# Optimization experiments

Measured on AMD Instinct MI355X. Metric: run time of the kernel, lower is better.

The kernel has to match this reference:

```python
import jax, jax.numpy as jnp
import numpy as np
from jax import lax

T = 0.2  # temperature

def _l2norm(x, axis):
    n = jnp.sqrt(jnp.sum(x * x, axis=axis, keepdims=True))
    return x / jnp.maximum(n, 1e-12)

def setup_inputs() -> dict:
    key = jax.random.key(0)
    k1, k2, k3, k4 = jax.random.split(key, 4)
    B, K, C, H, W, Q = 16, 5, 256, 128, 128, 64
    res1 = jax.random.normal(k1, (B, K, H, W), jnp.float32)
    fea1 = jax.random.normal(k2, (B, C, H, W), jnp.float32)
    gt = jax.random.randint(k3, (B, H, W), 0, K, dtype=jnp.int32)
    # queue buffers, L2-normalized along feature dim (torch normalize(dim=0) on [C,Q])
    queues = _l2norm(jax.random.normal(k4, (K, C, Q), jnp.float32), axis=1)
    return {"res1": res1, "fea1": fea1, "queues": queues, "gt": gt, "label_bs": 8}

def reference(res1, fea1, queues, gt, label_bs):
    B, K, H, W = res1.shape
    C = fea1.shape[1]
    HW = H * W
    # per-sample prediction: gt for labeled samples, argmax of logits otherwise
    pred_arg = jnp.argmax(res1, axis=1).reshape(B, HW)
    pred_gt = gt.reshape(B, HW).astype(pred_arg.dtype)
    labeled = (jnp.arange(B) < label_bs)[:, None]
    pred = jnp.where(labeled, pred_gt, pred_arg)  # [B, HW]

    fea = fea1.reshape(B, C, HW)
    # masked segment-mean per class (vectorized version of the per-unique-label loop)
    onehot = (pred[:, None, :] == jnp.arange(K)[None, :, None]).astype(fea.dtype)  # [B,K,HW]
    counts = onehot.sum(-1)                                    # [B,K]
    sums = jnp.einsum('bkp,bcp->bkc', onehot, fea)             # [B,K,C]
    means = sums / jnp.maximum(counts, 1.0)[..., None]
    keys_all = _l2norm(means, axis=-1)                         # [B,K,C]

    present = counts > 0                                       # [B,K]
    # Faithful replication of the source's off-by-one: keys[list(vals).index(c)]
    # selects the mean of the PREVIOUS present class (vals excludes the smallest
    # present label while keys keeps all unique labels in sorted order).
    idx = jnp.where(present, jnp.arange(K)[None, :], -1)
    cmax = lax.cummax(idx, axis=1)
    prev = jnp.concatenate([jnp.full((B, 1), -1, cmax.dtype), cmax[:, :-1]], axis=1)  # [B,K]
    smallest = jnp.argmax(present, axis=1)                     # first present class
    valid = present & (jnp.arange(K)[None, :] != smallest[:, None]) & (prev >= 0)

    query = jnp.take_along_axis(keys_all, jnp.maximum(prev, 0)[:, :, None], axis=1)  # [B,K,C]

    qd = lax.stop_gradient(queues)  # queues are detached buffers in the original
    sim = jnp.einsum('bkc,jcq->bkjq', query, qd) / T           # [B,K,K,Q]
    l_pos = jnp.einsum('bkc,kcq->bkq', query, qd) / T          # [B,K,Q]
    sumE = jnp.exp(sim).sum(-1)                                # [B,K,K]
    off = 1.0 - jnp.eye(K, dtype=sumE.dtype)
    neg = (sumE * off[None]).sum(-1)                           # [B,K] cross-class negatives
    l_neg = jnp.exp(l_pos) + neg[:, :, None]                   # [B,K,Q]
    log_prob = (l_pos - jnp.log(l_neg)).mean(-1)               # [B,K]

    loss_c = jnp.where(valid, -log_prob, 0.0)
    n_present = present.sum(1)
    denom = n_present - 1  # len(vals)
    per_sample = jnp.where(denom > 0, loss_c.sum(1) / jnp.maximum(denom, 1), 0.0)
    return per_sample.sum() / B
```

## Files before the change

kernel.cpp:

```cpp
#include <hip/hip_runtime.h>
#include <cstddef>

constexpr int B_  = 16;
constexpr int K_  = 5;
constexpr int C_  = 256;
constexpr int HW_ = 128 * 128;
constexpr int Q_  = 64;
constexpr float T_ = 0.2f;

typedef float f4 __attribute__((ext_vector_type(4)));

__global__ __launch_bounds__(256) void pred_kernel(
    const float* __restrict__ res1, const int* __restrict__ gt,
    const int* __restrict__ label_bs, unsigned int* __restrict__ predp)
{
    int idx = blockIdx.x * 256 + threadIdx.x;
    int b  = idx >> 12;
    int p4 = idx & 4095;
    int lb = label_bs[0];
    unsigned int packed;
    if (b < lb) {
        int4 g = reinterpret_cast<const int4*>(gt + (size_t)b * HW_)[p4];
        packed = (unsigned)(g.x & 0xFF) | ((unsigned)(g.y & 0xFF) << 8)
               | ((unsigned)(g.z & 0xFF) << 16) | ((unsigned)(g.w & 0xFF) << 24);
    } else {
        const float4* r = reinterpret_cast<const float4*>(res1 + (size_t)b * K_ * HW_) + p4;
        float4 best = r[0];
        int a0 = 0, a1 = 0, a2 = 0, a3 = 0;
        #pragma unroll
        for (int k = 1; k < K_; ++k) {
            float4 v = r[(size_t)k * (HW_ / 4)];
            if (v.x > best.x) { best.x = v.x; a0 = k; }
            if (v.y > best.y) { best.y = v.y; a1 = k; }
            if (v.z > best.z) { best.z = v.z; a2 = k; }
            if (v.w > best.w) { best.w = v.w; a3 = k; }
        }
        packed = (unsigned)a0 | ((unsigned)a1 << 8) | ((unsigned)a2 << 16) | ((unsigned)a3 << 24);
    }
    predp[idx] = packed;
}

__global__ __launch_bounds__(256) void segsum_kernel(
    const float* __restrict__ fea, const unsigned int* __restrict__ predp,
    float* __restrict__ sums, float* __restrict__ counts)
{
    int bc = blockIdx.x;
    int b = bc >> 8;
    int c = bc & (C_ - 1);
    int tid = threadIdx.x;
    const f4* frow = reinterpret_cast<const f4*>(fea + ((size_t)b * C_ + c) * HW_);
    const unsigned int* prow = predp + (size_t)b * (HW_ / 4);

    float acc[K_] = {};
    int   cnt[K_] = {};
    const bool do_count = (c == 0);

    for (int i = tid; i < HW_ / 4; i += 256) {
        f4 v = __builtin_nontemporal_load(frow + i);
        unsigned u = prow[i];
        int k0 = u & 255, k1 = (u >> 8) & 255, k2 = (u >> 16) & 255, k3 = u >> 24;
        #pragma unroll
        for (int k = 0; k < K_; ++k) {
            acc[k] += (k0 == k ? v.x : 0.f)
                    + (k1 == k ? v.y : 0.f)
                    + (k2 == k ? v.z : 0.f)
                    + (k3 == k ? v.w : 0.f);
        }
        if (do_count) {
            #pragma unroll
            for (int k = 0; k < K_; ++k)
                cnt[k] += (k0 == k) + (k1 == k) + (k2 == k) + (k3 == k);
        }
    }

    __shared__ float red[4][K_];
    __shared__ int   redc[4][K_];
    int lane = tid & 63, wv = tid >> 6;
    #pragma unroll
    for (int k = 0; k < K_; ++k) {
        float v = acc[k];
        #pragma unroll
        for (int off = 32; off > 0; off >>= 1) v += __shfl_down(v, off);
        if (lane == 0) red[wv][k] = v;
        if (do_count) {
            int ci = cnt[k];
            #pragma unroll
            for (int off = 32; off > 0; off >>= 1) ci += __shfl_down(ci, off);
            if (lane == 0) redc[wv][k] = ci;
        }
    }
    __syncthreads();
    if (tid < K_) {
        sums[((size_t)b * K_ + tid) * C_ + c] =
            red[0][tid] + red[1][tid] + red[2][tid] + red[3][tid];
        if (do_count)
            counts[b * K_ + tid] =
                (float)(redc[0][tid] + redc[1][tid] + redc[2][tid] + redc[3][tid]);
    }
}

__global__ __launch_bounds__(256) void loss_kernel(
    const float* __restrict__ sums, const float* __restrict__ counts,
    const float* __restrict__ queues, float* __restrict__ logprob)
{
    int bk = blockIdx.x;
    int b = bk / K_;
    int k = bk - b * K_;
    int tid = threadIdx.x, lane = tid & 63, wv = tid >> 6;

    __shared__ float key[C_];
    __shared__ float wred[4];
    __shared__ float sumE_s[K_];
    __shared__ float lpos_s[Q_];

    float cv[K_];
    #pragma unroll
    for (int j = 0; j < K_; ++j) cv[j] = counts[b * K_ + j];
    int prev = -1;
    #pragma unroll
    for (int j = 0; j < K_; ++j)
        if (j < k && cv[j] > 0.0f) prev = j;
    int pk = prev < 0 ? 0 : prev;

    float m = sums[((size_t)b * K_ + pk) * C_ + tid] / fmaxf(cv[pk], 1.0f);
    float s = m * m;
    #pragma unroll
    for (int off = 32; off > 0; off >>= 1) s += __shfl_down(s, off);
    if (lane == 0) wred[wv] = s;
    __syncthreads();
    float nrm = sqrtf(wred[0] + wred[1] + wred[2] + wred[3]);
    key[tid] = m / fmaxf(nrm, 1e-12f);
    __syncthreads();

    for (int j = wv; j < K_; j += 4) {
        const float* qj = queues + (size_t)j * C_ * Q_ + lane;
        float acc = 0.f;
        for (int c = 0; c < C_; ++c)
            acc += key[c] * qj[(size_t)c * Q_];
        acc = acc / T_;
        float e = expf(acc);
        float se = e;
        #pragma unroll
        for (int off = 32; off > 0; off >>= 1) se += __shfl_down(se, off);
        if (lane == 0) sumE_s[j] = se;
        if (j == k) lpos_s[lane] = acc;
    }
    __syncthreads();

    if (wv == 0) {
        float neg = 0.f;
        #pragma unroll
        for (int j = 0; j < K_; ++j)
            if (j != k) neg += sumE_s[j];
        float lp = lpos_s[lane];
        float term = lp - logf(expf(lp) + neg);
        #pragma unroll
        for (int off = 32; off > 0; off >>= 1) term += __shfl_down(term, off);
        if (lane == 0) logprob[bk] = term * (1.0f / (float)Q_);
    }
}

__global__ __launch_bounds__(64) void final_kernel(
    const float* __restrict__ counts, const float* __restrict__ logprob,
    float* __restrict__ out)
{
    int tid = threadIdx.x;
    float per = 0.f;
    if (tid < B_) {
        int last = -1, smallest = -1, npres = 0;
        float lsum = 0.f;
        #pragma unroll
        for (int k = 0; k < K_; ++k) {
            bool pres = counts[tid * K_ + k] > 0.0f;
            bool valid = pres && smallest >= 0 && last >= 0;
            if (valid) lsum += -logprob[tid * K_ + k];
            if (pres && smallest < 0) smallest = k;
            if (pres) { ++npres; last = k; }
        }
        int denom = npres - 1;
        per = (denom > 0) ? (lsum / (float)denom) : 0.f;
    }
    #pragma unroll
    for (int off = 32; off > 0; off >>= 1) per += __shfl_down(per, off);
    if (tid == 0) out[0] = per / (float)B_;
}

extern "C" void kernel_launch(void* const* d_in, const int* in_sizes, int n_in,
                              void* d_out, int out_size, void* d_ws, size_t ws_size,
                              hipStream_t stream)
{
    const float* res1     = (const float*)d_in[0];
    const float* fea1     = (const float*)d_in[1];
    const float* queues   = (const float*)d_in[2];
    const int*   gt       = (const int*)d_in[3];
    const int*   label_bs = (const int*)d_in[4];
    float* out = (float*)d_out;

    char* ws = (char*)d_ws;
    unsigned int* predp = (unsigned int*)ws;
    float* sums    = (float*)(ws + (size_t)B_ * (HW_ / 4) * 4);
    float* counts  = sums + (size_t)B_ * K_ * C_;
    float* logprob = counts + B_ * K_;

    pred_kernel<<<B_ * HW_ / 4 / 256, 256, 0, stream>>>(res1, gt, label_bs, predp);
    segsum_kernel<<<B_ * C_, 256, 0, stream>>>(fea1, predp, sums, counts);
    loss_kernel<<<B_ * K_, 256, 0, stream>>>(sums, counts, queues, logprob);
    final_kernel<<<1, 64, 0, stream>>>(counts, logprob, out);
}
```

Baseline: 64.50 us.

## Move class counting into pred kernel, fuse final reduction via last-block atomic

Class counts are now accumulated with atomics in the prediction kernel instead of in one channel's segsum block. The final reduction is folded into the loss kernel through a last-block-done atomic counter, which removes one launch but adds a memset launch. Segsum blocks now each process two (b,c) rows, halving the grid to 2048 blocks, with an unrolled inner loop. The main target is the launch overhead and load imbalance of a memory-bound pipeline that streams 268 MB of features.

```diff
diff --git a/kernel.cpp b/kernel.cpp
--- a/kernel.cpp
+++ b/kernel.cpp
@@ -12,96 +12,103 @@
 
 __global__ __launch_bounds__(256) void pred_kernel(
     const float* __restrict__ res1, const int* __restrict__ gt,
-    const int* __restrict__ label_bs, unsigned int* __restrict__ predp)
+    const int* __restrict__ label_bs, unsigned int* __restrict__ predp,
+    int* __restrict__ counts_i)
 {
     int idx = blockIdx.x * 256 + threadIdx.x;
     int b  = idx >> 12;
     int p4 = idx & 4095;
     int lb = label_bs[0];
-    unsigned int packed;
+    int k0, k1, k2, k3;
     if (b < lb) {
         int4 g = reinterpret_cast<const int4*>(gt + (size_t)b * HW_)[p4];
-        packed = (unsigned)(g.x & 0xFF) | ((unsigned)(g.y & 0xFF) << 8)
-               | ((unsigned)(g.z & 0xFF) << 16) | ((unsigned)(g.w & 0xFF) << 24);
+        k0 = g.x; k1 = g.y; k2 = g.z; k3 = g.w;
     } else {
         const float4* r = reinterpret_cast<const float4*>(res1 + (size_t)b * K_ * HW_) + p4;
         float4 best = r[0];
-        int a0 = 0, a1 = 0, a2 = 0, a3 = 0;
+        k0 = k1 = k2 = k3 = 0;
         #pragma unroll
         for (int k = 1; k < K_; ++k) {
             float4 v = r[(size_t)k * (HW_ / 4)];
-            if (v.x > best.x) { best.x = v.x; a0 = k; }
-            if (v.y > best.y) { best.y = v.y; a1 = k; }
-            if (v.z > best.z) { best.z = v.z; a2 = k; }
-            if (v.w > best.w) { best.w = v.w; a3 = k; }
-        }
-        packed = (unsigned)a0 | ((unsigned)a1 << 8) | ((unsigned)a2 << 16) | ((unsigned)a3 << 24);
-    }
-    predp[idx] = packed;
+            if (v.x > best.x) { best.x = v.x; k0 = k; }
+            if (v.y > best.y) { best.y = v.y; k1 = k; }
+            if (v.z > best.z) { best.z = v.z; k2 = k; }
+            if (v.w > best.w) { best.w = v.w; k3 = k; }
+        }
+    }
+    predp[idx] = (unsigned)k0 | ((unsigned)k1 << 8) | ((unsigned)k2 << 16) | ((unsigned)k3 << 24);
+
+    int cnt[K_];
+    #pragma unroll
+    for (int k = 0; k < K_; ++k)
+        cnt[k] = (k0 == k) + (k1 == k) + (k2 == k) + (k3 == k);
+
+    int lane = threadIdx.x & 63, wv = threadIdx.x >> 6;
+    __shared__ int redc[4][K_];
+    #pragma unroll
+    for (int k = 0; k < K_; ++k) {
+        int v = cnt[k];
+        #pragma unroll
+        for (int off = 32; off > 0; off >>= 1) v += __shfl_down(v, off);
+        if (lane == 0) redc[wv][k] = v;
+    }
+    __syncthreads();
+    if (threadIdx.x < K_)
+        atomicAdd(&counts_i[b * K_ + threadIdx.x],
+                  redc[0][threadIdx.x] + redc[1][threadIdx.x] +
+                  redc[2][threadIdx.x] + redc[3][threadIdx.x]);
 }
 
 __global__ __launch_bounds__(256) void segsum_kernel(
     const float* __restrict__ fea, const unsigned int* __restrict__ predp,
-    float* __restrict__ sums, float* __restrict__ counts)
-{
-    int bc = blockIdx.x;
-    int b = bc >> 8;
-    int c = bc & (C_ - 1);
+    float* __restrict__ sums)
+{
     int tid = threadIdx.x;
-    const f4* frow = reinterpret_cast<const f4*>(fea + ((size_t)b * C_ + c) * HW_);
-    const unsigned int* prow = predp + (size_t)b * (HW_ / 4);
-
-    float acc[K_] = {};
-    int   cnt[K_] = {};
-    const bool do_count = (c == 0);
-
-    for (int i = tid; i < HW_ / 4; i += 256) {
-        f4 v = __builtin_nontemporal_load(frow + i);
-        unsigned u = prow[i];
-        int k0 = u & 255, k1 = (u >> 8) & 255, k2 = (u >> 16) & 255, k3 = u >> 24;
+    int lane = tid & 63, wv = tid >> 6;
+    __shared__ float red[4][K_];
+
+    #pragma unroll
+    for (int r = 0; r < 2; ++r) {
+        int bc = blockIdx.x + r * 2048;
+        int b = bc >> 8;
+        int c = bc & (C_ - 1);
+        const f4* frow = reinterpret_cast<const f4*>(fea + ((size_t)b * C_ + c) * HW_);
+        const unsigned int* prow = predp + (size_t)b * (HW_ / 4);
+
+        float acc[K_] = {};
+        #pragma unroll 4
+        for (int i = tid; i < HW_ / 4; i += 256) {
+            f4 v = __builtin_nontemporal_load(frow + i);
+            unsigned u = prow[i];
+            int k0 = u & 255, k1 = (u >> 8) & 255, k2 = (u >> 16) & 255, k3 = u >> 24;
+            #pragma unroll
+            for (int k = 0; k < K_; ++k) {
+                acc[k] += (k0 == k ? v.x : 0.f)
+                        + (k1 == k ? v.y : 0.f)
+                        + (k2 == k ? v.z : 0.f)
+                        + (k3 == k ? v.w : 0.f);
+            }
+        }
+
         #pragma unroll
         for (int k = 0; k < K_; ++k) {
-            acc[k] += (k0 == k ? v.x : 0.f)
-                    + (k1 == k ? v.y : 0.f)
-                    + (k2 == k ? v.z : 0.f)
-                    + (k3 == k ? v.w : 0.f);
-        }
-        if (do_count) {
+            float v = acc[k];
             #pragma unroll
-            for (int k = 0; k < K_; ++k)
-                cnt[k] += (k0 == k) + (k1 == k) + (k2 == k) + (k3 == k);
-        }
-    }
-
-    __shared__ float red[4][K_];
-    __shared__ int   redc[4][K_];
-    int lane = tid & 63, wv = tid >> 6;
-    #pragma unroll
-    for (int k = 0; k < K_; ++k) {
-        float v = acc[k];
-        #pragma unroll
-        for (int off = 32; off > 0; off >>= 1) v += __shfl_down(v, off);
-        if (lane == 0) red[wv][k] = v;
-        if (do_count) {
-            int ci = cnt[k];
-            #pragma unroll
-            for (int off = 32; off > 0; off >>= 1) ci += __shfl_down(ci, off);
-            if (lane == 0) redc[wv][k] = ci;
-        }
-    }
-    __syncthreads();
-    if (tid < K_) {
-        sums[((size_t)b * K_ + tid) * C_ + c] =
-            red[0][tid] + red[1][tid] + red[2][tid] + red[3][tid];
-        if (do_count)
-            counts[b * K_ + tid] =
-                (float)(redc[0][tid] + redc[1][tid] + redc[2][tid] + redc[3][tid]);
+            for (int off = 32; off > 0; off >>= 1) v += __shfl_down(v, off);
+            if (lane == 0) red[wv][k] = v;
+        }
+        __syncthreads();
+        if (tid < K_)
+            sums[((size_t)b * K_ + tid) * C_ + c] =
+                red[0][tid] + red[1][tid] + red[2][tid] + red[3][tid];
+        __syncthreads();
     }
 }
 
 __global__ __launch_bounds__(256) void loss_kernel(
-    const float* __restrict__ sums, const float* __restrict__ counts,
-    const float* __restrict__ queues, float* __restrict__ logprob)
+    const float* __restrict__ sums, const int* __restrict__ counts_i,
+    const float* __restrict__ queues, float* __restrict__ logprob,
+    int* __restrict__ flag, float* __restrict__ out)
 {
     int bk = blockIdx.x;
     int b = bk / K_;
@@ -112,17 +119,18 @@
     __shared__ float wred[4];
     __shared__ float sumE_s[K_];
     __shared__ float lpos_s[Q_];
-
-    float cv[K_];
-    #pragma unroll
-    for (int j = 0; j < K_; ++j) cv[j] = counts[b * K_ + j];
+    __shared__ int   last_s;
+
+    int cv[K_];
+    #pragma unroll
+    for (int j = 0; j < K_; ++j) cv[j] = counts_i[b * K_ + j];
     int prev = -1;
     #pragma unroll
     for (int j = 0; j < K_; ++j)
-        if (j < k && cv[j] > 0.0f) prev = j;
+        if (j < k && cv[j] > 0) prev = j;
     int pk = prev < 0 ? 0 : prev;
 
-    float m = sums[((size_t)b * K_ + pk) * C_ + tid] / fmaxf(cv[pk], 1.0f);
+    float m = sums[((size_t)b * K_ + pk) * C_ + tid] / fmaxf((float)cv[pk], 1.0f);
     float s = m * m;
     #pragma unroll
     for (int off = 32; off > 0; off >>= 1) s += __shfl_down(s, off);
@@ -158,31 +166,34 @@
         for (int off = 32; off > 0; off >>= 1) term += __shfl_down(term, off);
         if (lane == 0) logprob[bk] = term * (1.0f / (float)Q_);
     }
-}
-
-__global__ __launch_bounds__(64) void final_kernel(
-    const float* __restrict__ counts, const float* __restrict__ logprob,
-    float* __restrict__ out)
-{
-    int tid = threadIdx.x;
-    float per = 0.f;
-    if (tid < B_) {
-        int last = -1, smallest = -1, npres = 0;
-        float lsum = 0.f;
-        #pragma unroll
-        for (int k = 0; k < K_; ++k) {
-            bool pres = counts[tid * K_ + k] > 0.0f;
-            bool valid = pres && smallest >= 0 && last >= 0;
-            if (valid) lsum += -logprob[tid * K_ + k];
-            if (pres && smallest < 0) smallest = k;
-            if (pres) { ++npres; last = k; }
-        }
-        int denom = npres - 1;
-        per = (denom > 0) ? (lsum / (float)denom) : 0.f;
-    }
-    #pragma unroll
-    for (int off = 32; off > 0; off >>= 1) per += __shfl_down(per, off);
-    if (tid == 0) out[0] = per / (float)B_;
+    __syncthreads();
+
+    if (tid == 0) {
+        __threadfence();
+        last_s = (atomicAdd(flag, 1) == B_ * K_ - 1);
+    }
+    __syncthreads();
+    if (last_s && wv == 0) {
+        __threadfence();
+        float per = 0.f;
+        if (lane < B_) {
+            int last = -1, smallest = -1, npres = 0;
+            float lsum = 0.f;
+            #pragma unroll
+            for (int kk = 0; kk < K_; ++kk) {
+                bool pres = counts_i[lane * K_ + kk] > 0;
+                bool valid = pres && smallest >= 0 && last >= 0;
+                if (valid) lsum += -logprob[lane * K_ + kk];
+                if (pres && smallest < 0) smallest = kk;
+                if (pres) { ++npres; last = kk; }
+            }
+            int denom = npres - 1;
+            per = (denom > 0) ? (lsum / (float)denom) : 0.f;
+        }
+        #pragma unroll
+        for (int off = 32; off > 0; off >>= 1) per += __shfl_down(per, off);
+        if (lane == 0) out[0] = per / (float)B_;
+    }
 }
 
 extern "C" void kernel_launch(void* const* d_in, const int* in_sizes, int n_in,
@@ -198,12 +209,14 @@
 
     char* ws = (char*)d_ws;
     unsigned int* predp = (unsigned int*)ws;
-    float* sums    = (float*)(ws + (size_t)B_ * (HW_ / 4) * 4);
-    float* counts  = sums + (size_t)B_ * K_ * C_;
-    float* logprob = counts + B_ * K_;
-
-    pred_kernel<<<B_ * HW_ / 4 / 256, 256, 0, stream>>>(res1, gt, label_bs, predp);
-    segsum_kernel<<<B_ * C_, 256, 0, stream>>>(fea1, predp, sums, counts);
-    loss_kernel<<<B_ * K_, 256, 0, stream>>>(sums, counts, queues, logprob);
-    final_kernel<<<1, 64, 0, stream>>>(counts, logprob, out);
-}
+    float* sums     = (float*)(ws + (size_t)B_ * (HW_ / 4) * 4);
+    int*   counts_i = (int*)(sums + (size_t)B_ * K_ * C_);
+    int*   flag     = counts_i + B_ * K_;
+    float* logprob  = (float*)(flag + 1);
+
+    hipMemsetAsync(counts_i, 0, (B_ * K_ + 1) * sizeof(int), stream);
+
+    pred_kernel<<<B_ * HW_ / 4 / 256, 256, 0, stream>>>(res1, gt, label_bs, predp, counts_i);
+    segsum_kernel<<<2048, 256, 0, stream>>>(fea1, predp, sums);
+    loss_kernel<<<B_ * K_, 256, 0, stream>>>(sums, counts_i, queues, logprob, flag, out);
+}
```

Result: slower. 70.15 us (+8.8%).
